# Performance work log

Measured on AMD Instinct MI355X. Metric: run time of the kernel, lower is better.

## Reference

```python
import jax, jax.numpy as jnp
import numpy as np

N_NODES = 1024
BATCH = 64
N = N_NODES * BATCH          # 65536 total nodes
BBX, LBL = 7, 1
H1, H2, H3 = 512, 16, 4096
LAT = 512
NCLS = 160
N_EDGES = 262144


def setup_inputs() -> dict:
    key = jax.random.key(0)
    ks = jax.random.split(key, 20)
    g = lambda k, shape: (jax.random.normal(k, shape, jnp.float32) * 0.02)
    inp = dict(
        E=jax.random.randint(ks[0], (2, N_EDGES), 0, N, dtype=jnp.int64),
        X_data=jax.random.normal(ks[1], (N, BBX + LBL), jnp.float32),
        class_labels=jax.random.uniform(ks[2], (BATCH * NCLS,), jnp.float32),
        # GCNConv weights (no bias, no normalize, no self-loops)
        W_g1=g(ks[3], (BBX + LBL, H1)),
        W_g2=g(ks[4], (H1, H2)),
        # dense layers ([in, out] convention; y = x @ W + b)
        W_box=g(ks[5], (BBX, H2)), b_box=jnp.zeros((H2,), jnp.float32),
        W_lbl=g(ks[6], (LBL, H2)), b_lbl=jnp.zeros((H2,), jnp.float32),
        W_d1=g(ks[7], (H2 * N_NODES, H3)), b_d1=jnp.zeros((H3,), jnp.float32),
        W_d2=g(ks[8], (H2 * N_NODES + NCLS, H3)), b_d2=jnp.zeros((H3,), jnp.float32),
        W_d3=g(ks[9], (H3, H3)), b_d3=jnp.zeros((H3,), jnp.float32),
        W_z=g(ks[10], (H3, LAT)), b_z=jnp.zeros((LAT,), jnp.float32),
    )
    return inp


def reference(E, X_data, class_labels, W_g1, W_g2, W_box, b_box, W_lbl, b_lbl,
              W_d1, b_d1, W_d2, b_d2, W_d3, b_d3, W_z, b_z):
    relu = jax.nn.relu
    src, dst = E[0], E[1]
    # GCNConv (normalize=False, add_self_loops=False, bias=False):
    # out[i] = sum_{(j->i) in E} (x @ W)[j]
    x = jax.ops.segment_sum((X_data @ W_g1)[src], dst, num_segments=N)   # [N, H1]
    x = jax.ops.segment_sum((x @ W_g2)[src], dst, num_segments=N)        # [N, H2]
    x = x.reshape(BATCH, N_NODES * H2)                                   # [B, 16*num_nodes]
    boxes = relu(X_data[:, 1:].reshape(BATCH, N_NODES, BBX) @ W_box + b_box)
    labels = relu(X_data[:, :1].reshape(BATCH, N_NODES, LBL) @ W_lbl + b_lbl)
    mix = (boxes + labels).reshape(BATCH, N_NODES * H2)
    mix = relu(mix @ W_d1 + b_d1)                                        # [B, H3]
    cls = class_labels.reshape(BATCH, NCLS)
    x = jnp.concatenate([cls, x], axis=-1)                               # [B, NCLS + 16*num_nodes]
    x = relu(x @ W_d2 + b_d2)
    x = x + mix
    x = relu(x @ W_d3 + b_d3)
    x = relu(x @ W_d3 + b_d3)
    z_mean = relu(x @ W_z + b_z)
    z_logvar = relu(x @ W_z + b_z)
    return (z_mean, z_logvar)
```

## Files before the change

kernel.cpp:

```cpp
#include <hip/hip_runtime.h>
#include <stdint.h>

typedef unsigned short u16;
typedef short bf16x8 __attribute__((ext_vector_type(8)));
typedef short bf16x4 __attribute__((ext_vector_type(4)));
typedef float f32x4 __attribute__((ext_vector_type(4)));

#define NTOT   65536
#define NB     64
#define NEDGE  262144
#define H3     4096
#define LATD   512
#define NCLS_  160
#define K1     16384
#define K2     16544

static __device__ __forceinline__ u16 f2b(float f) {
  uint32_t x = __float_as_uint(f);
  return (u16)((x + 0x7FFFu + ((x >> 16) & 1u)) >> 16);
}

__global__ void k_hist(const int* __restrict__ E, int* __restrict__ cnt,
                       const float* __restrict__ Wg1, const float* __restrict__ Wg2,
                       float* __restrict__ Wc) {
  int e = blockIdx.x * 256 + threadIdx.x;
  atomicAdd(&cnt[E[NEDGE + e]], 1);
  if (blockIdx.x == 0 && threadIdx.x < 128) {
    int c = threadIdx.x >> 4, h = threadIdx.x & 15;
    float acc = 0.f;
    for (int k = 0; k < 512; ++k) acc += Wg1[c * 512 + k] * Wg2[k * 16 + h];
    Wc[c * 16 + h] = acc;
  }
}

__global__ __launch_bounds__(1024) void k_scan(const int* __restrict__ cnt,
                                               int* __restrict__ off,
                                               int* __restrict__ cur) {
  __shared__ int wsum[16];
  const int t = threadIdx.x;
  const int lane = t & 63, w = t >> 6;
  const int base = t << 6;
  int s = 0;
  const int4* c4 = (const int4*)(cnt + base);
  #pragma unroll 4
  for (int i = 0; i < 16; ++i) { int4 v = c4[i]; s += v.x + v.y + v.z + v.w; }
  int sc = s;
  #pragma unroll
  for (int d = 1; d < 64; d <<= 1) {
    int u = __shfl_up(sc, d);
    if (lane >= d) sc += u;
  }
  if (lane == 63) wsum[w] = sc;
  __syncthreads();
  if (w == 0 && lane < 16) {
    int v = wsum[lane];
    #pragma unroll
    for (int d = 1; d < 16; d <<= 1) {
      int u = __shfl_up(v, d);
      if (lane >= d) v += u;
    }
    wsum[lane] = v;
  }
  __syncthreads();
  int run = (w == 0 ? 0 : wsum[w - 1]) + (sc - s);
  int4* o4 = (int4*)(off + base);
  int4* u4 = (int4*)(cur + base);
  #pragma unroll 4
  for (int i = 0; i < 16; ++i) {
    int4 v = c4[i];
    int4 r;
    r.x = run; run += v.x;
    r.y = run; run += v.y;
    r.z = run; run += v.z;
    r.w = run; run += v.w;
    o4[i] = r; u4[i] = r;
  }
}

__global__ void k_scatter(const int* __restrict__ E, int* __restrict__ cur,
                          int* __restrict__ csr) {
  int e = blockIdx.x * 256 + threadIdx.x;
  int p = atomicAdd(&cur[E[NEDGE + e]], 1);
  csr[p] = E[e];
}

__global__ void k_gather(const int* __restrict__ off, const int* __restrict__ cnt,
                         const int* __restrict__ csr, const float* __restrict__ In,
                         float* __restrict__ Out) {
  int t = blockIdx.x * 256 + threadIdx.x;
  int n = t >> 3, c = t & 7;
  int b = off[n], e = b + cnt[n];
  float acc = 0.f;
  for (int j = b; j < e; ++j) acc += In[(size_t)csr[j] * 8 + c];
  Out[(size_t)n * 8 + c] = acc;
}

__global__ void k_nodes(const float* __restrict__ S2, const float* __restrict__ Wc,
                        const float* __restrict__ X,
                        const float* __restrict__ Wbox, const float* __restrict__ bbox,
                        const float* __restrict__ Wlbl, const float* __restrict__ blbl,
                        const float* __restrict__ cls,
                        u16* __restrict__ Abuf, u16* __restrict__ Mbuf) {
  int idx = blockIdx.x * 256 + threadIdx.x;
  if (idx < NB * NCLS_) {
    int m = idx / NCLS_, i = idx - m * NCLS_;
    Abuf[(size_t)m * K2 + i] = f2b(cls[idx]);
  }
  if (idx >= NTOT * 16) return;
  int n = idx >> 4, h = idx & 15;
  int m = n >> 10, nl = n & 1023;
  const float* s2 = S2 + (size_t)n * 8;
  float xg = 0.f;
  #pragma unroll
  for (int c = 0; c < 8; ++c) xg += s2[c] * Wc[c * 16 + h];
  Abuf[(size_t)m * K2 + 160 + nl * 16 + h] = f2b(xg);
  const float* xr = X + (size_t)n * 8;
  float box = bbox[h];
  #pragma unroll
  for (int c = 0; c < 7; ++c) box += xr[1 + c] * Wbox[c * 16 + h];
  box = box > 0.f ? box : 0.f;
  float lb = xr[0] * Wlbl[h] + blbl[h];
  lb = lb > 0.f ? lb : 0.f;
  Mbuf[(size_t)m * K1 + nl * 16 + h] = f2b(box + lb);
}

__device__ __forceinline__ void gl16(const void* g, void* l) {
  __builtin_amdgcn_global_load_lds(
      (const __attribute__((address_space(1))) unsigned int*)g,
      (__attribute__((address_space(3))) unsigned int*)l, 16, 0, 0);
}

__global__ __launch_bounds__(256) void k_gemm(
    const u16* __restrict__ A0, const u16* __restrict__ A1, int lda0, int lda1,
    const float* __restrict__ W0, const float* __restrict__ W1, int Nw,
    int tot0, int tot1, int per0, int per1, int slabBase1,
    float* __restrict__ Cs)
{
  __shared__ u16 ldsA[2048];
  __shared__ u16 ldsWT[2048];

  const u16* A; int lda; const float* W; int tot, per, slab;
  if (blockIdx.z == 0) { A = A0; lda = lda0; W = W0; tot = tot0; per = per0; slab = blockIdx.y; }
  else                 { A = A1; lda = lda1; W = W1; tot = tot1; per = per1; slab = slabBase1 + blockIdx.y; }

  const int n0  = blockIdx.x << 6;
  const int sp0 = blockIdx.y * per;
  int ns = tot - sp0; if (ns > per) ns = per;
  if (ns <= 0) return;
  const int t  = threadIdx.x;
  const int l  = t & 63;
  const int wv = t >> 6;

  const int rA  = t >> 2;
  const int cAg = (t & 3) ^ ((rA >> 1) & 3);
  const u16* gA = A + (size_t)rA * lda + cAg * 8 + (size_t)sp0 * 32;
  u16* lA = &ldsA[t * 8];

  const int q  = t >> 5;
  const int nc = (t & 31) * 2;
  const int mW = (t & 31) & 3;
  const float* gW = W + (size_t)(sp0 * 32 + 4 * q) * Nw + n0 + nc;
  u16* lwt0 = &ldsWT[nc * 32 + ((4 * q) ^ (8 * mW))];
  u16* lwt1 = lwt0 + 32;
  const size_t stepW = (size_t)32 * Nw;

  const int rAf  = (wv << 4) + (l & 15);
  const int aoff = rAf * 32 + (((l >> 4) ^ ((rAf >> 1) & 3)) << 3);
  const int g4 = l >> 4;
  const int li = l & 15;
  const int mR = (li >> 1) & 3;
  const int fo = li * 32 + 8 * (g4 ^ mR);

  f32x4 ac0 = {0.f, 0.f, 0.f, 0.f}, ac1 = ac0, ac2 = ac0, ac3 = ac0;

  float2 wr0 = *(const float2*)(gW);
  float2 wr1 = *(const float2*)(gW + Nw);
  float2 wr2 = *(const float2*)(gW + 2 * Nw);
  float2 wr3 = *(const float2*)(gW + 3 * Nw);

  for (int st = 0; st < ns; ++st) {
    __syncthreads();
    bf16x4 p0 = { (short)f2b(wr0.x), (short)f2b(wr1.x), (short)f2b(wr2.x), (short)f2b(wr3.x) };
    bf16x4 p1 = { (short)f2b(wr0.y), (short)f2b(wr1.y), (short)f2b(wr2.y), (short)f2b(wr3.y) };
    *(bf16x4*)lwt0 = p0;
    *(bf16x4*)lwt1 = p1;
    gl16(gA + (size_t)st * 32, lA);
    __syncthreads();
    const float* gWn = gW + (st + 1 < ns ? (size_t)(st + 1) * stepW : (size_t)st * stepW);
    wr0 = *(const float2*)(gWn);
    wr1 = *(const float2*)(gWn + Nw);
    wr2 = *(const float2*)(gWn + 2 * Nw);
    wr3 = *(const float2*)(gWn + 3 * Nw);

    bf16x8 a  = *(const bf16x8*)(&ldsA[aoff]);
    bf16x8 b0 = *(const bf16x8*)(&ldsWT[fo]);
    bf16x8 b1 = *(const bf16x8*)(&ldsWT[fo + 512]);
    bf16x8 b2 = *(const bf16x8*)(&ldsWT[fo + 1024]);
    bf16x8 b3 = *(const bf16x8*)(&ldsWT[fo + 1536]);
    ac0 = __builtin_amdgcn_mfma_f32_16x16x32_bf16(a, b0, ac0, 0, 0, 0);
    ac1 = __builtin_amdgcn_mfma_f32_16x16x32_bf16(a, b1, ac1, 0, 0, 0);
    ac2 = __builtin_amdgcn_mfma_f32_16x16x32_bf16(a, b2, ac2, 0, 0, 0);
    ac3 = __builtin_amdgcn_mfma_f32_16x16x32_bf16(a, b3, ac3, 0, 0, 0);
  }

  const int col  = n0 + li;
  const int row0 = (wv << 4) + (g4 << 2);
  float* base = Cs + (size_t)slab * NB * Nw;
  #pragma unroll
  for (int j = 0; j < 4; ++j) {
    float* cp = base + (size_t)(row0 + j) * Nw + col;
    cp[0]  = ac0[j];
    cp[16] = ac1[j];
    cp[32] = ac2[j];
    cp[48] = ac3[j];
  }
}

__global__ void k_ep12(const float* __restrict__ Cs,
                       const float* __restrict__ b1, const float* __restrict__ b2,
                       u16* __restrict__ A3) {
  int i = blockIdx.x * 256 + threadIdx.x;
  if (i >= NB * H3) return;
  float mix = b1[i & (H3 - 1)];
  float v   = b2[i & (H3 - 1)];
  #pragma unroll 4
  for (int s = 0; s < 16; ++s)  mix += Cs[(size_t)s * (NB * H3) + i];
  #pragma unroll 4
  for (int s = 16; s < 32; ++s) v   += Cs[(size_t)s * (NB * H3) + i];
  mix = mix > 0.f ? mix : 0.f;
  v   = v   > 0.f ? v   : 0.f;
  A3[i] = f2b(v + mix);
}

__global__ void k_ep(const float* __restrict__ Cs, int nslab, int slabElems,
                     const float* __restrict__ bias, u16* __restrict__ outb,
                     int colmask, int total) {
  int i = blockIdx.x * 256 + threadIdx.x;
  if (i >= total) return;
  float v = bias[i & colmask];
  #pragma unroll 4
  for (int s = 0; s < nslab; ++s) v += Cs[(size_t)s * slabElems + i];
  v = v > 0.f ? v : 0.f;
  outb[i] = f2b(v);
}

__global__ void k_ep5(const float* __restrict__ Cs, int nslab,
                      const float* __restrict__ bz, float* __restrict__ out) {
  int i = blockIdx.x * 256 + threadIdx.x;
  if (i >= NB * LATD) return;
  float v = bz[i & 511];
  #pragma unroll 4
  for (int s = 0; s < nslab; ++s) v += Cs[(size_t)s * (NB * LATD) + i];
  v = v > 0.f ? v : 0.f;
  out[i] = v;
  out[NB * LATD + i] = v;
}

extern "C" void kernel_launch(void* const* d_in, const int* in_sizes, int n_in,
                              void* d_out, int out_size, void* d_ws, size_t ws_size,
                              hipStream_t stream) {
  const int*   E    = (const int*)d_in[0];
  const float* X    = (const float*)d_in[1];
  const float* cls  = (const float*)d_in[2];
  const float* Wg1  = (const float*)d_in[3];
  const float* Wg2  = (const float*)d_in[4];
  const float* Wbox = (const float*)d_in[5];
  const float* bbox = (const float*)d_in[6];
  const float* Wlbl = (const float*)d_in[7];
  const float* blbl = (const float*)d_in[8];
  const float* Wd1  = (const float*)d_in[9];
  const float* bd1  = (const float*)d_in[10];
  const float* Wd2  = (const float*)d_in[11];
  const float* bd2  = (const float*)d_in[12];
  const float* Wd3  = (const float*)d_in[13];
  const float* bd3  = (const float*)d_in[14];
  const float* Wz   = (const float*)d_in[15];
  const float* bz   = (const float*)d_in[16];

  char* ws = (char*)d_ws;
  int*   cnt  = (int*)  (ws + 0x000000);
  int*   off  = (int*)  (ws + 0x040000);
  int*   cur  = (int*)  (ws + 0x080000);
  int*   csr  = (int*)  (ws + 0x0C0000);
  float* S1   = (float*)(ws + 0x1C0000);
  float* S2   = (float*)(ws + 0x3C0000);
  float* Wc   = (float*)(ws + 0x5C0000);
  u16*   A3   = (u16*)  (ws + 0x5C1000);
  u16*   A4   = (u16*)  (ws + 0x641000);
  u16*   A5   = (u16*)  (ws + 0x6C1000);
  u16*   Mbuf = (u16*)  (ws + 0x741000);
  u16*   Abuf = (u16*)  (ws + 0x941000);
  float* Cslb = (float*)(ws + 0xB50000);

  hipMemsetAsync(cnt, 0, 0x40000, stream);
  k_hist   <<<NEDGE / 256, 256, 0, stream>>>(E, cnt, Wg1, Wg2, Wc);
  k_scan   <<<1, 1024, 0, stream>>>(cnt, off, cur);
  k_scatter<<<NEDGE / 256, 256, 0, stream>>>(E, cur, csr);
  k_gather <<<NTOT * 8 / 256, 256, 0, stream>>>(off, cnt, csr, X,  S1);
  k_gather <<<NTOT * 8 / 256, 256, 0, stream>>>(off, cnt, csr, S1, S2);
  k_nodes  <<<NTOT * 16 / 256, 256, 0, stream>>>(S2, Wc, X, Wbox, bbox, Wlbl, blbl,
                                                 cls, Abuf, Mbuf);

  { dim3 g(64, 16, 2);
    k_gemm<<<g, 256, 0, stream>>>(Mbuf, Abuf, K1, K2, Wd1, Wd2, H3,
                                  512, 517, 32, 33, 16, Cslb); }
  k_ep12<<<NB * H3 / 256, 256, 0, stream>>>(Cslb, bd1, bd2, A3);

  { dim3 g(64, 16, 1);
    k_gemm<<<g, 256, 0, stream>>>(A3, A3, H3, H3, Wd3, Wd3, H3,
                                  128, 128, 8, 8, 0, Cslb); }
  k_ep<<<NB * H3 / 256, 256, 0, stream>>>(Cslb, 16, NB * H3, bd3, A4, H3 - 1, NB * H3);

  { dim3 g(64, 16, 1);
    k_gemm<<<g, 256, 0, stream>>>(A4, A4, H3, H3, Wd3, Wd3, H3,
                                  128, 128, 8, 8, 0, Cslb); }
  k_ep<<<NB * H3 / 256, 256, 0, stream>>>(Cslb, 16, NB * H3, bd3, A5, H3 - 1, NB * H3);

  { dim3 g(8, 32, 1);
    k_gemm<<<g, 256, 0, stream>>>(A5, A5, H3, H3, Wz, Wz, LATD,
                                  128, 128, 4, 4, 0, Cslb); }
  k_ep5<<<NB * LATD / 256, 256, 0, stream>>>(Cslb, 32, bz, (float*)d_out);
}
```

Baseline: 307.7 us.

## Double-buffer LDS tiles in split-K GEMM with one barrier per step

The GEMM main loop moves from a single LDS buffer with two __syncthreads per K-step to ping-pong A and W buffers. The next A tile is fetched into LDS asynchronously and the next-next W registers are prefetched while the MFMAs run, with manual waitcnt and one s_barrier per step. The aim is to overlap global loads with compute and halve barrier stalls, at the cost of double the LDS use and hand-tuned vmcnt counts that must stay correct.

```diff
diff --git a/kernel.cpp b/kernel.cpp
--- a/kernel.cpp
+++ b/kernel.cpp
@@ -130,14 +130,48 @@
       (__attribute__((address_space(3))) unsigned int*)l, 16, 0, 0);
 }
 
+#define GEMM_STEP(ST, ArD, WrD, AwR, WwR)                                      \
+  {                                                                            \
+    const int i1 = (ST) + 1 < ns ? (ST) + 1 : ns - 1;                          \
+    const int i2 = (ST) + 2 < ns ? (ST) + 2 : ns - 1;                          \
+    gl16(gA + (size_t)i1 * 32, &AwR[t * 8]);                                   \
+    __builtin_amdgcn_sched_barrier(0);                                         \
+    bf16x8 a  = *(const bf16x8*)(&ArD[aoff]);                                  \
+    bf16x8 b0 = *(const bf16x8*)(&WrD[fo]);                                    \
+    bf16x8 b1 = *(const bf16x8*)(&WrD[fo + 512]);                              \
+    bf16x8 b2 = *(const bf16x8*)(&WrD[fo + 1024]);                             \
+    bf16x8 b3 = *(const bf16x8*)(&WrD[fo + 1536]);                             \
+    bf16x4 p0 = { (short)f2b(wr0.x), (short)f2b(wr1.x),                        \
+                  (short)f2b(wr2.x), (short)f2b(wr3.x) };                      \
+    bf16x4 p1 = { (short)f2b(wr0.y), (short)f2b(wr1.y),                        \
+                  (short)f2b(wr2.y), (short)f2b(wr3.y) };                      \
+    *(bf16x4*)(&WwR[wtOff0]) = p0;                                             \
+    *(bf16x4*)(&WwR[wtOff1]) = p1;                                             \
+    const float* gWn = gW + (size_t)i2 * stepW;                                \
+    wr0 = *(const float2*)(gWn);                                               \
+    wr1 = *(const float2*)(gWn + Nw);                                          \
+    wr2 = *(const float2*)(gWn + 2 * Nw);                                      \
+    wr3 = *(const float2*)(gWn + 3 * Nw);                                      \
+    ac0 = __builtin_amdgcn_mfma_f32_16x16x32_bf16(a, b0, ac0, 0, 0, 0);        \
+    ac1 = __builtin_amdgcn_mfma_f32_16x16x32_bf16(a, b1, ac1, 0, 0, 0);        \
+    ac2 = __builtin_amdgcn_mfma_f32_16x16x32_bf16(a, b2, ac2, 0, 0, 0);        \
+    ac3 = __builtin_amdgcn_mfma_f32_16x16x32_bf16(a, b3, ac3, 0, 0, 0);        \
+    asm volatile("s_waitcnt lgkmcnt(0)" ::: "memory");                         \
+    asm volatile("s_waitcnt vmcnt(4)" ::: "memory");                           \
+    __builtin_amdgcn_s_barrier();                                              \
+    asm volatile("" ::: "memory");                                             \
+  }
+
 __global__ __launch_bounds__(256) void k_gemm(
     const u16* __restrict__ A0, const u16* __restrict__ A1, int lda0, int lda1,
     const float* __restrict__ W0, const float* __restrict__ W1, int Nw,
     int tot0, int tot1, int per0, int per1, int slabBase1,
     float* __restrict__ Cs)
 {
-  __shared__ u16 ldsA[2048];
-  __shared__ u16 ldsWT[2048];
+  __shared__ u16 lA0[2048];
+  __shared__ u16 lA1[2048];
+  __shared__ u16 lW0[2048];
+  __shared__ u16 lW1[2048];
 
   const u16* A; int lda; const float* W; int tot, per, slab;
   if (blockIdx.z == 0) { A = A0; lda = lda0; W = W0; tot = tot0; per = per0; slab = blockIdx.y; }
@@ -154,14 +188,13 @@
   const int rA  = t >> 2;
   const int cAg = (t & 3) ^ ((rA >> 1) & 3);
   const u16* gA = A + (size_t)rA * lda + cAg * 8 + (size_t)sp0 * 32;
-  u16* lA = &ldsA[t * 8];
 
   const int q  = t >> 5;
   const int nc = (t & 31) * 2;
   const int mW = (t & 31) & 3;
   const float* gW = W + (size_t)(sp0 * 32 + 4 * q) * Nw + n0 + nc;
-  u16* lwt0 = &ldsWT[nc * 32 + ((4 * q) ^ (8 * mW))];
-  u16* lwt1 = lwt0 + 32;
+  const int wtOff0 = nc * 32 + ((4 * q) ^ (8 * mW));
+  const int wtOff1 = wtOff0 + 32;
   const size_t stepW = (size_t)32 * Nw;
 
   const int rAf  = (wv << 4) + (l & 15);
@@ -173,34 +206,39 @@
 
   f32x4 ac0 = {0.f, 0.f, 0.f, 0.f}, ac1 = ac0, ac2 = ac0, ac3 = ac0;
 
-  float2 wr0 = *(const float2*)(gW);
-  float2 wr1 = *(const float2*)(gW + Nw);
-  float2 wr2 = *(const float2*)(gW + 2 * Nw);
-  float2 wr3 = *(const float2*)(gW + 3 * Nw);
-
-  for (int st = 0; st < ns; ++st) {
-    __syncthreads();
-    bf16x4 p0 = { (short)f2b(wr0.x), (short)f2b(wr1.x), (short)f2b(wr2.x), (short)f2b(wr3.x) };
-    bf16x4 p1 = { (short)f2b(wr0.y), (short)f2b(wr1.y), (short)f2b(wr2.y), (short)f2b(wr3.y) };
-    *(bf16x4*)lwt0 = p0;
-    *(bf16x4*)lwt1 = p1;
-    gl16(gA + (size_t)st * 32, lA);
-    __syncthreads();
-    const float* gWn = gW + (st + 1 < ns ? (size_t)(st + 1) * stepW : (size_t)st * stepW);
+  float2 wr0, wr1, wr2, wr3;
+  gl16(gA, &lA0[t * 8]);
+  __builtin_amdgcn_sched_barrier(0);
+  wr0 = *(const float2*)(gW);
+  wr1 = *(const float2*)(gW + Nw);
+  wr2 = *(const float2*)(gW + 2 * Nw);
+  wr3 = *(const float2*)(gW + 3 * Nw);
+  {
+    bf16x4 p0 = { (short)f2b(wr0.x), (short)f2b(wr1.x),
+                  (short)f2b(wr2.x), (short)f2b(wr3.x) };
+    bf16x4 p1 = { (short)f2b(wr0.y), (short)f2b(wr1.y),
+                  (short)f2b(wr2.y), (short)f2b(wr3.y) };
+    *(bf16x4*)(&lW0[wtOff0]) = p0;
+    *(bf16x4*)(&lW0[wtOff1]) = p1;
+    const int i1p = 1 < ns ? 1 : 0;
+    const float* gWn = gW + (size_t)i1p * stepW;
     wr0 = *(const float2*)(gWn);
     wr1 = *(const float2*)(gWn + Nw);
     wr2 = *(const float2*)(gWn + 2 * Nw);
     wr3 = *(const float2*)(gWn + 3 * Nw);
-
-    bf16x8 a  = *(const bf16x8*)(&ldsA[aoff]);
-    bf16x8 b0 = *(const bf16x8*)(&ldsWT[fo]);
-    bf16x8 b1 = *(const bf16x8*)(&ldsWT[fo + 512]);
-    bf16x8 b2 = *(const bf16x8*)(&ldsWT[fo + 1024]);
-    bf16x8 b3 = *(const bf16x8*)(&ldsWT[fo + 1536]);
-    ac0 = __builtin_amdgcn_mfma_f32_16x16x32_bf16(a, b0, ac0, 0, 0, 0);
-    ac1 = __builtin_amdgcn_mfma_f32_16x16x32_bf16(a, b1, ac1, 0, 0, 0);
-    ac2 = __builtin_amdgcn_mfma_f32_16x16x32_bf16(a, b2, ac2, 0, 0, 0);
-    ac3 = __builtin_amdgcn_mfma_f32_16x16x32_bf16(a, b3, ac3, 0, 0, 0);
+  }
+  asm volatile("s_waitcnt lgkmcnt(0)" ::: "memory");
+  asm volatile("s_waitcnt vmcnt(4)" ::: "memory");
+  __builtin_amdgcn_s_barrier();
+  asm volatile("" ::: "memory");
+
+  int st = 0;
+  for (; st + 2 <= ns; st += 2) {
+    GEMM_STEP(st,     lA0, lW0, lA1, lW1);
+    GEMM_STEP(st + 1, lA1, lW1, lA0, lW0);
+  }
+  if (st < ns) {
+    GEMM_STEP(st, lA0, lW0, lA1, lW1);
   }
 
   const int col  = n0 + li;
```

After: 309.0 us. About the same (+0.4%).

## Widen GEMM tile to 256 columns with double-buffered LDS and register prefetch

Applied to the files above, without the earlier changes.

The split-K GEMM now computes a 64x256 output tile per block instead of 64x64. Each wave owns 64 columns and holds 16 accumulators. A and W tiles are double-buffered in LDS, with a two-step-ahead register prefetch and a single barrier per k-step. The fp32-to-bf16 conversion of weights uses packed v_cvt_pk_bf16_f32 and 16-byte LDS stores. This cuts the grid by 4x, which raises per-block reuse of A but lowers parallelism and adds register and LDS pressure.

```diff
diff --git a/kernel.cpp b/kernel.cpp
--- a/kernel.cpp
+++ b/kernel.cpp
@@ -124,11 +124,68 @@
   Mbuf[(size_t)m * K1 + nl * 16 + h] = f2b(box + lb);
 }
 
-__device__ __forceinline__ void gl16(const void* g, void* l) {
-  __builtin_amdgcn_global_load_lds(
-      (const __attribute__((address_space(1))) unsigned int*)g,
-      (__attribute__((address_space(3))) unsigned int*)l, 16, 0, 0);
-}
+#define CVTPK(dst, lo, hi) \
+  asm("v_cvt_pk_bf16_f32 %0, %1, %2" : "=v"(dst) : "v"(lo), "v"(hi))
+
+#define WPACK(I2, WwR)                                                         \
+  { const int n_ = (l << 2) + (I2);                                            \
+    const int sw_ = ((n_ >> 1) ^ (n_ >> 2)) & 3;                               \
+    uint32_t q0, q1, q2, q3;                                                   \
+    CVTPK(q0, ws0[I2], ws1[I2]);                                               \
+    CVTPK(q1, ws2[I2], ws3[I2]);                                               \
+    CVTPK(q2, ws4[I2], ws5[I2]);                                               \
+    CVTPK(q3, ws6[I2], ws7[I2]);                                               \
+    uint4 pk_ = {q0, q1, q2, q3};                                              \
+    *(uint4*)(&WwR[n_ * 32 + ((wv ^ sw_) << 3)]) = pk_; }
+
+#define WLOADS(II)                                                             \
+  { const float* gw_ = gW + (size_t)(II) * stepW;                              \
+    ws0 = *(const f32x4*)(gw_);                                                \
+    ws1 = *(const f32x4*)(gw_ + Nw);                                           \
+    ws2 = *(const f32x4*)(gw_ + 2 * Nw);                                       \
+    ws3 = *(const f32x4*)(gw_ + 3 * Nw);                                       \
+    ws4 = *(const f32x4*)(gw_ + 4 * Nw);                                       \
+    ws5 = *(const f32x4*)(gw_ + 5 * Nw);                                       \
+    ws6 = *(const f32x4*)(gw_ + 6 * Nw);                                       \
+    ws7 = *(const f32x4*)(gw_ + 7 * Nw);                                       \
+    aS  = *(const int4*)(gA + (size_t)(II) * 32); }
+
+#define MFMA_BF16 __builtin_amdgcn_mfma_f32_16x16x32_bf16
+
+#define GEMM_STEP(ST, ArD, WrD, AwR, WwR)                                      \
+  {                                                                            \
+    bf16x8 a0 = *(const bf16x8*)(&ArD[foA]);                                   \
+    bf16x8 a1 = *(const bf16x8*)(&ArD[foA + 512]);                             \
+    bf16x8 a2 = *(const bf16x8*)(&ArD[foA + 1024]);                            \
+    bf16x8 a3 = *(const bf16x8*)(&ArD[foA + 1536]);                            \
+    bf16x8 b0 = *(const bf16x8*)(&WrD[foB]);                                   \
+    bf16x8 b1 = *(const bf16x8*)(&WrD[foB + 512]);                             \
+    bf16x8 b2 = *(const bf16x8*)(&WrD[foB + 1024]);                            \
+    bf16x8 b3 = *(const bf16x8*)(&WrD[foB + 1536]);                            \
+    *(int4*)(&AwR[t * 8]) = aS;                                                \
+    WPACK(0, WwR) WPACK(1, WwR) WPACK(2, WwR) WPACK(3, WwR)                    \
+    { const int ii = (ST) + 2 < ns ? (ST) + 2 : ns - 1;                        \
+      WLOADS(ii) }                                                             \
+    acc00 = MFMA_BF16(a0, b0, acc00, 0, 0, 0);                                 \
+    acc01 = MFMA_BF16(a0, b1, acc01, 0, 0, 0);                                 \
+    acc02 = MFMA_BF16(a0, b2, acc02, 0, 0, 0);                                 \
+    acc03 = MFMA_BF16(a0, b3, acc03, 0, 0, 0);                                 \
+    acc10 = MFMA_BF16(a1, b0, acc10, 0, 0, 0);                                 \
+    acc11 = MFMA_BF16(a1, b1, acc11, 0, 0, 0);                                 \
+    acc12 = MFMA_BF16(a1, b2, acc12, 0, 0, 0);                                 \
+    acc13 = MFMA_BF16(a1, b3, acc13, 0, 0, 0);                                 \
+    acc20 = MFMA_BF16(a2, b0, acc20, 0, 0, 0);                                 \
+    acc21 = MFMA_BF16(a2, b1, acc21, 0, 0, 0);                                 \
+    acc22 = MFMA_BF16(a2, b2, acc22, 0, 0, 0);                                 \
+    acc23 = MFMA_BF16(a2, b3, acc23, 0, 0, 0);                                 \
+    acc30 = MFMA_BF16(a3, b0, acc30, 0, 0, 0);                                 \
+    acc31 = MFMA_BF16(a3, b1, acc31, 0, 0, 0);                                 \
+    acc32 = MFMA_BF16(a3, b2, acc32, 0, 0, 0);                                 \
+    acc33 = MFMA_BF16(a3, b3, acc33, 0, 0, 0);                                 \
+    asm volatile("s_waitcnt lgkmcnt(0)" ::: "memory");                         \
+    __builtin_amdgcn_s_barrier();                                              \
+    asm volatile("" ::: "memory");                                             \
+  }
 
 __global__ __launch_bounds__(256) void k_gemm(
     const u16* __restrict__ A0, const u16* __restrict__ A1, int lda0, int lda1,
@@ -136,14 +193,16 @@
     int tot0, int tot1, int per0, int per1, int slabBase1,
     float* __restrict__ Cs)
 {
-  __shared__ u16 ldsA[2048];
-  __shared__ u16 ldsWT[2048];
+  __shared__ u16 lA0[2048];
+  __shared__ u16 lA1[2048];
+  __shared__ u16 lW0[8192];
+  __shared__ u16 lW1[8192];
 
   const u16* A; int lda; const float* W; int tot, per, slab;
   if (blockIdx.z == 0) { A = A0; lda = lda0; W = W0; tot = tot0; per = per0; slab = blockIdx.y; }
   else                 { A = A1; lda = lda1; W = W1; tot = tot1; per = per1; slab = slabBase1 + blockIdx.y; }
 
-  const int n0  = blockIdx.x << 6;
+  const int n0  = blockIdx.x << 8;
   const int sp0 = blockIdx.y * per;
   int ns = tot - sp0; if (ns > per) ns = per;
   if (ns <= 0) return;
@@ -154,65 +213,66 @@
   const int rA  = t >> 2;
   const int cAg = (t & 3) ^ ((rA >> 1) & 3);
   const u16* gA = A + (size_t)rA * lda + cAg * 8 + (size_t)sp0 * 32;
-  u16* lA = &ldsA[t * 8];
-
-  const int q  = t >> 5;
-  const int nc = (t & 31) * 2;
-  const int mW = (t & 31) & 3;
-  const float* gW = W + (size_t)(sp0 * 32 + 4 * q) * Nw + n0 + nc;
-  u16* lwt0 = &ldsWT[nc * 32 + ((4 * q) ^ (8 * mW))];
-  u16* lwt1 = lwt0 + 32;
+
+  const float* gW = W + (size_t)(sp0 * 32 + wv * 8) * Nw + n0 + l * 4;
   const size_t stepW = (size_t)32 * Nw;
 
-  const int rAf  = (wv << 4) + (l & 15);
-  const int aoff = rAf * 32 + (((l >> 4) ^ ((rAf >> 1) & 3)) << 3);
   const int g4 = l >> 4;
   const int li = l & 15;
-  const int mR = (li >> 1) & 3;
-  const int fo = li * 32 + 8 * (g4 ^ mR);
-
-  f32x4 ac0 = {0.f, 0.f, 0.f, 0.f}, ac1 = ac0, ac2 = ac0, ac3 = ac0;
-
-  float2 wr0 = *(const float2*)(gW);
-  float2 wr1 = *(const float2*)(gW + Nw);
-  float2 wr2 = *(const float2*)(gW + 2 * Nw);
-  float2 wr3 = *(const float2*)(gW + 3 * Nw);
-
-  for (int st = 0; st < ns; ++st) {
-    __syncthreads();
-    bf16x4 p0 = { (short)f2b(wr0.x), (short)f2b(wr1.x), (short)f2b(wr2.x), (short)f2b(wr3.x) };
-    bf16x4 p1 = { (short)f2b(wr0.y), (short)f2b(wr1.y), (short)f2b(wr2.y), (short)f2b(wr3.y) };
-    *(bf16x4*)lwt0 = p0;
-    *(bf16x4*)lwt1 = p1;
-    gl16(gA + (size_t)st * 32, lA);
-    __syncthreads();
-    const float* gWn = gW + (st + 1 < ns ? (size_t)(st + 1) * stepW : (size_t)st * stepW);
-    wr0 = *(const float2*)(gWn);
-    wr1 = *(const float2*)(gWn + Nw);
-    wr2 = *(const float2*)(gWn + 2 * Nw);
-    wr3 = *(const float2*)(gWn + 3 * Nw);
-
-    bf16x8 a  = *(const bf16x8*)(&ldsA[aoff]);
-    bf16x8 b0 = *(const bf16x8*)(&ldsWT[fo]);
-    bf16x8 b1 = *(const bf16x8*)(&ldsWT[fo + 512]);
-    bf16x8 b2 = *(const bf16x8*)(&ldsWT[fo + 1024]);
-    bf16x8 b3 = *(const bf16x8*)(&ldsWT[fo + 1536]);
-    ac0 = __builtin_amdgcn_mfma_f32_16x16x32_bf16(a, b0, ac0, 0, 0, 0);
-    ac1 = __builtin_amdgcn_mfma_f32_16x16x32_bf16(a, b1, ac1, 0, 0, 0);
-    ac2 = __builtin_amdgcn_mfma_f32_16x16x32_bf16(a, b2, ac2, 0, 0, 0);
-    ac3 = __builtin_amdgcn_mfma_f32_16x16x32_bf16(a, b3, ac3, 0, 0, 0);
-  }
-
-  const int col  = n0 + li;
-  const int row0 = (wv << 4) + (g4 << 2);
-  float* base = Cs + (size_t)slab * NB * Nw;
+  const int foA = li * 32 + ((g4 ^ ((li >> 1) & 3)) << 3);
+  const int foB = wv * 2048 + li * 32 +
+                  ((g4 ^ (((li >> 1) ^ (li >> 2)) & 3)) << 3);
+
+  f32x4 z4 = {0.f, 0.f, 0.f, 0.f};
+  f32x4 acc00 = z4, acc01 = z4, acc02 = z4, acc03 = z4;
+  f32x4 acc10 = z4, acc11 = z4, acc12 = z4, acc13 = z4;
+  f32x4 acc20 = z4, acc21 = z4, acc22 = z4, acc23 = z4;
+  f32x4 acc30 = z4, acc31 = z4, acc32 = z4, acc33 = z4;
+
+  f32x4 ws0, ws1, ws2, ws3, ws4, ws5, ws6, ws7;
+  int4 aS;
+
+  WLOADS(0)
+  *(int4*)(&lA0[t * 8]) = aS;
+  WPACK(0, lW0) WPACK(1, lW0) WPACK(2, lW0) WPACK(3, lW0)
+  { const int i1 = 1 < ns ? 1 : 0;
+    WLOADS(i1) }
+  asm volatile("s_waitcnt lgkmcnt(0)" ::: "memory");
+  __builtin_amdgcn_s_barrier();
+  asm volatile("" ::: "memory");
+
+  int st = 0;
+  for (; st + 2 <= ns; st += 2) {
+    GEMM_STEP(st,     lA0, lW0, lA1, lW1)
+    GEMM_STEP(st + 1, lA1, lW1, lA0, lW0)
+  }
+  if (st < ns) {
+    GEMM_STEP(st, lA0, lW0, lA1, lW1)
+  }
+
+  float* base = Cs + (size_t)slab * NB * Nw + n0 + wv * 64 + li;
   #pragma unroll
   for (int j = 0; j < 4; ++j) {
-    float* cp = base + (size_t)(row0 + j) * Nw + col;
-    cp[0]  = ac0[j];
-    cp[16] = ac1[j];
-    cp[32] = ac2[j];
-    cp[48] = ac3[j];
+    float* r0 = base + (size_t)(g4 * 4 + j) * Nw;
+    r0[0]                    = acc00[j];
+    r0[16]                   = acc01[j];
+    r0[32]                   = acc02[j];
+    r0[48]                   = acc03[j];
+    float* r1 = r0 + 16 * Nw;
+    r1[0]                    = acc10[j];
+    r1[16]                   = acc11[j];
+    r1[32]                   = acc12[j];
+    r1[48]                   = acc13[j];
+    float* r2 = r0 + 32 * Nw;
+    r2[0]                    = acc20[j];
+    r2[16]                   = acc21[j];
+    r2[32]                   = acc22[j];
+    r2[48]                   = acc23[j];
+    float* r3 = r0 + 48 * Nw;
+    r3[0]                    = acc30[j];
+    r3[16]                   = acc31[j];
+    r3[32]                   = acc32[j];
+    r3[48]                   = acc33[j];
   }
 }
 
@@ -301,22 +361,22 @@
   k_nodes  <<<NTOT * 16 / 256, 256, 0, stream>>>(S2, Wc, X, Wbox, bbox, Wlbl, blbl,
                                                  cls, Abuf, Mbuf);
 
-  { dim3 g(64, 16, 2);
+  { dim3 g(16, 16, 2);
     k_gemm<<<g, 256, 0, stream>>>(Mbuf, Abuf, K1, K2, Wd1, Wd2, H3,
                                   512, 517, 32, 33, 16, Cslb); }
   k_ep12<<<NB * H3 / 256, 256, 0, stream>>>(Cslb, bd1, bd2, A3);
 
-  { dim3 g(64, 16, 1);
+  { dim3 g(16, 16, 1);
     k_gemm<<<g, 256, 0, stream>>>(A3, A3, H3, H3, Wd3, Wd3, H3,
                                   128, 128, 8, 8, 0, Cslb); }
   k_ep<<<NB * H3 / 256, 256, 0, stream>>>(Cslb, 16, NB * H3, bd3, A4, H3 - 1, NB * H3);
 
-  { dim3 g(64, 16, 1);
+  { dim3 g(16, 16, 1);
     k_gemm<<<g, 256, 0, stream>>>(A4, A4, H3, H3, Wd3, Wd3, H3,
                                   128, 128, 8, 8, 0, Cslb); }
   k_ep<<<NB * H3 / 256, 256, 0, stream>>>(Cslb, 16, NB * H3, bd3, A5, H3 - 1, NB * H3);
 
-  { dim3 g(8, 32, 1);
+  { dim3 g(2, 32, 1);
     k_gemm<<<g, 256, 0, stream>>>(A5, A5, H3, H3, Wz, Wz, LATD,
                                   128, 128, 4, 4, 0, Cslb); }
   k_ep5<<<NB * LATD / 256, 256, 0, stream>>>(Cslb, 32, bz, (float*)d_out);
```

Result: faster. 296.7 us (-3.6%).
